# Performance work log

Hardware: AMD Instinct MI355X
Metric: run time of the kernel (lower is better)

The kernel has to match this reference:

```python
import jax, jax.numpy as jnp
import numpy as np

N_TAU = 100  # number of steps per delay interval: dt = tau / N_TAU = 0.01 * tau


def _F(x, y, t, params):
    # Delay-logistic vector field: x'(t) = theta0 * x(t) * (1 - theta1 * x(t - tau))
    return params[0] * x * (1.0 - params[1] * y)


def setup_inputs() -> dict:
    key = jax.random.key(0)
    k1, = jax.random.split(key, 1)
    d = 32768
    x_0 = jax.random.uniform(k1, (d,), dtype=jnp.float32)  # positive ICs, stable dynamics
    tau = jnp.ones((1,), dtype=jnp.float32)
    params = jnp.ones((2,), dtype=jnp.float32)  # theta0, theta1
    N = 1000  # T = N * dt = 10 * tau
    return {"x_0": x_0, "tau": tau, "params": params, "N": N}


def reference(x_0, tau, params, N):
    # Forward-Euler DDE solve with constant history x(t) = x_0 for t in [-tau, 0].
    d = x_0.shape[0]
    dt = 0.01 * tau[0]
    dtype = x_0.dtype
    traj0 = jnp.zeros((N + 1, d), dtype=dtype).at[0].set(x_0)  # rows are time steps

    def step(traj, i):
        x_i = traj[i]                                            # current state [d]
        # delayed state x(t_i - tau): history (= x_0) for the first N_TAU steps
        y_i = jnp.where(i >= N_TAU, traj[jnp.maximum(i - N_TAU, 0)], x_0)
        t_i = i.astype(dtype) * dt
        x_next = x_i + dt * _F(x_i, y_i, t_i, params)
        return traj.at[i + 1].set(x_next), None

    traj, _ = jax.lax.scan(step, traj0, jnp.arange(N))
    # match torch convention: kth COLUMN is the state at the kth time step -> [d, N+1]
    return traj.T
```

## Files before the change

### kernel.cpp

```cpp
#include <hip/hip_runtime.h>


constexpr int NT   = 1000;
constexpr int NTAU = 100;
constexpr int NGRP = NT / NTAU;
constexpr int NP1  = NT + 1;
constexpr int COMP = 64;
constexpr int LSTR = NTAU + 1;
constexpr int NCW  = 3;

#define R5(F,B)   F(B) F((B)+1) F((B)+2) F((B)+3) F((B)+4)
#define R25(F,B)  R5(F,B) R5(F,(B)+5) R5(F,(B)+10) R5(F,(B)+15) R5(F,(B)+20)
#define R50(F,B)  R25(F,B) R25(F,(B)+25)
#define R100(F)   R50(F,0) R50(F,50)

__global__ __launch_bounds__(256, 1)
void ndde_kernel(const float* __restrict__ x0,
                 const float* __restrict__ tau,
                 const float* __restrict__ params,
                 float* __restrict__ out)
{
    __shared__ float buf[2][COMP][LSTR];
    const int tid  = threadIdx.x;
    const int wid  = tid >> 6;
    const int lane = tid & 63;
    const int jbase = (int)blockIdx.x * COMP;

    const float dt = 0.01f * tau[0];
    const float a  = dt * params[0];
    const float q  = -(a * params[1]);
    const float p  = 1.0f + a;

    float x = 0.0f;
    float h[NTAU];
#define STEP(K) { const float y_ = h[(K)]; h[(K)] = x; x *= fmaf(q, y_, p); }

    if (wid == 0) {
        x = x0[jbase + lane];
#define INIT_H(K) h[(K)] = x;
        R100(INIT_H)
        R100(STEP)
        float* bp = &buf[0][lane][0];
#define STG(K) bp[(K)] = h[(K)];
        R100(STG)
    }
    __syncthreads();

    for (int g = 0; g < NGRP; ++g) {
        if (wid == 0) {
            if (g + 1 < NGRP) {
                R100(STEP)
                float* bp = &buf[(g + 1) & 1][lane][0];
                R100(STG)
            }
        } else {
            const float* bb = &buf[g & 1][0][0];
            float* gp = out + jbase * NP1 + g * NTAU + lane;
            for (int r = wid - 1; r < COMP; r += NCW) {
                const float* lr = bb + r * LSTR;
                float* rp = gp + r * NP1;
                rp[0] = lr[lane];
                if (lane < NTAU - 64)
                    rp[64] = lr[64 + lane];
            }
        }
        __syncthreads();
    }

    if (wid == 0)
        out[(jbase + lane) * NP1 + NT] = x;
}

extern "C" void kernel_launch(void* const* d_in, const int* in_sizes, int n_in,
                              void* d_out, int out_size, void* d_ws, size_t ws_size,
                              hipStream_t stream) {
    const float* x0     = (const float*)d_in[0];
    const float* tau    = (const float*)d_in[1];
    const float* params = (const float*)d_in[2];
    float* out = (float*)d_out;
    const int d = in_sizes[0];
    const int nblocks = d / COMP;
    ndde_kernel<<<nblocks, 256, 0, stream>>>(x0, tau, params, out);
}
```

Baseline: 32.49 us.

## Replace block barriers with LDS flag producer-consumer handshake between waves

Swaps the per-group __syncthreads between the compute wave and the three store waves for shared-memory progress counters that waves poll with s_sleep. The producer waits only until every consumer has finished reading the buffer it is about to overwrite, and each consumer waits only for the producer's flag. This decouples the waves so the serial recurrence is not held back by the slowest store wave at every group. In exchange it adds spin-polling, explicit lgkmcnt waits, and a dependence on wave-level memory ordering within the block being correct.

```diff
diff --git a/kernel.cpp b/kernel.cpp
--- a/kernel.cpp
+++ b/kernel.cpp
@@ -14,6 +14,12 @@
 #define R50(F,B)  R25(F,B) R25(F,(B)+25)
 #define R100(F)   R50(F,0) R50(F,50)
 
+#define LDS_ORDER() do {                                    \
+    __builtin_amdgcn_sched_barrier(0);                      \
+    asm volatile("s_waitcnt lgkmcnt(0)" ::: "memory");      \
+    __builtin_amdgcn_sched_barrier(0);                      \
+} while (0)
+
 __global__ __launch_bounds__(256, 1)
 void ndde_kernel(const float* __restrict__ x0,
                  const float* __restrict__ tau,
@@ -21,6 +27,8 @@
                  float* __restrict__ out)
 {
     __shared__ float buf[2][COMP][LSTR];
+    __shared__ int   prodf;
+    __shared__ int   consf[NCW];
     const int tid  = threadIdx.x;
     const int wid  = tid >> 6;
     const int lane = tid & 63;
@@ -31,44 +39,55 @@
     const float q  = -(a * params[1]);
     const float p  = 1.0f + a;
 
-    float x = 0.0f;
-    float h[NTAU];
-#define STEP(K) { const float y_ = h[(K)]; h[(K)] = x; x *= fmaf(q, y_, p); }
+    if (tid == 0) { prodf = 0; consf[0] = 0; consf[1] = 0; consf[2] = 0; }
+    __syncthreads();
+
+    volatile int* vprod = &prodf;
+    volatile int* vcons = consf;
 
     if (wid == 0) {
-        x = x0[jbase + lane];
+        float x = x0[jbase + lane];
+        float h[NTAU];
 #define INIT_H(K) h[(K)] = x;
         R100(INIT_H)
-        R100(STEP)
-        float* bp = &buf[0][lane][0];
-#define STG(K) bp[(K)] = h[(K)];
-        R100(STG)
-    }
-    __syncthreads();
+#define STEP(K) { const float y_ = h[(K)]; h[(K)] = x; x *= fmaf(q, y_, p); }
+#define STG(K)  bp[(K)] = h[(K)];
 
-    for (int g = 0; g < NGRP; ++g) {
-        if (wid == 0) {
-            if (g + 1 < NGRP) {
-                R100(STEP)
-                float* bp = &buf[(g + 1) & 1][lane][0];
-                R100(STG)
+#pragma clang loop unroll(disable)
+        for (int g = 0; g < NGRP; ++g) {
+            if (g >= 2) {
+                while (vcons[0] < g - 1 || vcons[1] < g - 1 || vcons[2] < g - 1)
+                    __builtin_amdgcn_s_sleep(1);
+                LDS_ORDER();
             }
-        } else {
+            R100(STEP)
+            float* bp = &buf[g & 1][lane][0];
+            R100(STG)
+            LDS_ORDER();
+            *vprod = g + 1;
+        }
+        out[(jbase + lane) * NP1 + NT] = x;
+    } else {
+        const int cw = wid - 1;
+        float* gpb = out + jbase * NP1 + lane;
+#pragma clang loop unroll(disable)
+        for (int g = 0; g < NGRP; ++g) {
+            while (*vprod < g + 1)
+                __builtin_amdgcn_s_sleep(1);
+            LDS_ORDER();
             const float* bb = &buf[g & 1][0][0];
-            float* gp = out + jbase * NP1 + g * NTAU + lane;
-            for (int r = wid - 1; r < COMP; r += NCW) {
+            float* gp = gpb + g * NTAU;
+            for (int r = cw; r < COMP; r += NCW) {
                 const float* lr = bb + r * LSTR;
                 float* rp = gp + r * NP1;
                 rp[0] = lr[lane];
                 if (lane < NTAU - 64)
                     rp[64] = lr[64 + lane];
             }
+            LDS_ORDER();
+            vcons[cw] = g + 1;
         }
-        __syncthreads();
     }
-
-    if (wid == 0)
-        out[(jbase + lane) * NP1 + NT] = x;
 }
 
 extern "C" void kernel_launch(void* const* d_in, const int* in_sizes, int n_in,
```

New measurement: 33.21 us. 2.2% more time.
